# Kernel tuning notes

Measured on AMD Instinct MI355X. Metric: run time of the kernel, lower is better.

Reference implementation:

```python
import jax, jax.numpy as jnp
import numpy as np

# Config (matches init_kwargs)
N_HEAD, D_K, D_MODEL, D_INNER, N_LAYERS = 8, 64, 512, 2048, 4
VOCAB, PAD_IDX, REP_IDX, N_POSITION = 512, 0, 1, 200
B, N_NEAR, S = 64, 32, 12  # B batches, 32 near-POIs each, <=12 type tokens per POI
NPOI = B * N_NEAR


def sinusoid_table(n_position, d):
    pos = np.arange(n_position)[:, None].astype(np.float64)
    i = np.arange(d)[None, :]
    angle = pos / np.power(10000.0, 2 * (i // 2) / d)
    tab = np.zeros((n_position, d))
    tab[:, 0::2] = np.sin(angle[:, 0::2])
    tab[:, 1::2] = np.cos(angle[:, 1::2])
    return jnp.asarray(tab, jnp.float32)


def layer_norm(x, g, b, eps=1e-6):
    m = jnp.mean(x, -1, keepdims=True)
    v = jnp.var(x, -1, keepdims=True)
    return g * (x - m) * jax.lax.rsqrt(v + eps) + b


def pack_indices(npl, ttn):
    """Replace the torch Python-loop ragged pack with a single precomputed gather.
    Returns per-output-slot (poi_idx, tok_idx) and a validity mask [B, L]."""
    npl = np.asarray(npl); ttn = np.asarray(ttn)
    Bn = len(npl)
    ends = np.cumsum(npl); starts = ends - npl
    seq_len = np.array([1 + int(ttn[starts[b]:ends[b]].sum()) for b in range(Bn)])
    L = int(seq_len.max())  # == max_batch_len in the torch code
    poi_idx = np.zeros((Bn, L), np.int32)
    tok_idx = np.zeros((Bn, L), np.int32)
    for b in range(Bn):
        pos = 1  # slot 0 is the [REP] token
        for p in range(int(starts[b]), int(ends[b])):
            t = int(ttn[p])
            poi_idx[b, pos:pos + t] = p
            tok_idx[b, pos:pos + t] = np.arange(t)
            pos += t
    valid = np.arange(L)[None, :] < seq_len[:, None]  # pad_from_num_list(pad_num)
    return poi_idx, tok_idx, valid


def setup_inputs() -> dict:
    key = jax.random.key(0)
    ks = jax.random.split(key, 24)
    nrm = lambda k, shape, s=0.02: jax.random.normal(k, shape, jnp.float32) * s
    poi_type = jax.random.randint(ks[0], (NPOI, S), 0, VOCAB, jnp.int32)
    loc_emb = jax.random.normal(ks[1], (NPOI, D_MODEL), jnp.float32)
    near_pois_num_list = jnp.full((B,), N_NEAR, jnp.int32)
    type_token_num = jax.random.randint(ks[2], (NPOI,), 1, S + 1, jnp.int32)
    emb = nrm(ks[3], (VOCAB, D_MODEL), 1.0).at[PAD_IDX].set(0.0)  # padding_idx row zeroed
    return {
        "poi_type": poi_type, "loc_emb": loc_emb,
        "near_pois_num_list": near_pois_num_list, "type_token_num": type_token_num,
        "emb": emb,
        "Wq": nrm(ks[4], (N_LAYERS, D_MODEL, D_MODEL)),
        "Wk": nrm(ks[5], (N_LAYERS, D_MODEL, D_MODEL)),
        "Wv": nrm(ks[6], (N_LAYERS, D_MODEL, D_MODEL)),
        "Wo": nrm(ks[7], (N_LAYERS, D_MODEL, D_MODEL)),
        "bo": jnp.zeros((N_LAYERS, D_MODEL), jnp.float32),
        "ln1_g": jnp.ones((N_LAYERS, D_MODEL), jnp.float32),
        "ln1_b": jnp.zeros((N_LAYERS, D_MODEL), jnp.float32),
        "W1": nrm(ks[8], (N_LAYERS, D_MODEL, D_INNER)),
        "b1": jnp.zeros((N_LAYERS, D_INNER), jnp.float32),
        "W2": nrm(ks[9], (N_LAYERS, D_INNER, D_MODEL)),
        "b2": jnp.zeros((N_LAYERS, D_MODEL), jnp.float32),
        "ln2_g": jnp.ones((N_LAYERS, D_MODEL), jnp.float32),
        "ln2_b": jnp.zeros((N_LAYERS, D_MODEL), jnp.float32),
        "lnf_g": jnp.ones((D_MODEL,), jnp.float32),
        "lnf_b": jnp.zeros((D_MODEL,), jnp.float32),
    }


def encoder_forward(poi_type, loc_emb, poi_idx, tok_idx, tok_mask, attn_mask,
                    emb, Wq, Wk, Wv, Wo, bo, ln1_g, ln1_b, W1, b1, W2, b2,
                    ln2_g, ln2_b, lnf_g, lnf_b):
    pos_table = sinusoid_table(N_POSITION, D_MODEL)
    # embedding + positional encoding (dropout = eval/identity) + location broadcast
    enc = emb[poi_type] + pos_table[None, :S, :] + loc_emb[:, None, :]  # [NPOI, S, D]
    # fused ragged gather+pad (replaces the per-row torch.cat loop)
    x = jnp.where(tok_mask[..., None], enc[poi_idx, tok_idx], 0.0)      # [B, L, D]
    x = x.at[:, 0, :].set(emb[REP_IDX])                                  # [REP] token at slot 0
    x = layer_norm(x, lnf_g, lnf_b)
    Bn, L, D = x.shape
    inv_temp = np.float32(1.0 / np.sqrt(D_K))
    for l in range(N_LAYERS):
        # multi-head self-attention, post-LN residual
        q = (x @ Wq[l]).reshape(Bn, L, N_HEAD, D_K)
        k = (x @ Wk[l]).reshape(Bn, L, N_HEAD, D_K)
        v = (x @ Wv[l]).reshape(Bn, L, N_HEAD, D_K)
        scores = jnp.einsum('bqhd,bkhd->bhqk', q, k) * inv_temp
        scores = jnp.where(attn_mask[:, None, None, :], scores, -1e9)
        attn = jax.nn.softmax(scores, axis=-1)
        o = jnp.einsum('bhqk,bkhd->bqhd', attn, v).reshape(Bn, L, D)
        x = layer_norm(x + o @ Wo[l] + bo[l], ln1_g[l], ln1_b[l])
        # position-wise FFN, post-LN residual
        h = jax.nn.relu(x @ W1[l] + b1[l])
        x = layer_norm(x + h @ W2[l] + b2[l], ln2_g[l], ln2_b[l])
    return x


def reference(poi_type, loc_emb, near_pois_num_list, type_token_num,
              emb, Wq, Wk, Wv, Wo, bo, ln1_g, ln1_b, W1, b1, W2, b2,
              ln2_g, ln2_b, lnf_g, lnf_b):
    poi_idx, tok_idx, valid = pack_indices(np.asarray(near_pois_num_list),
                                           np.asarray(type_token_num))
    L = valid.shape[1]
    tok_mask = jnp.asarray(valid & (np.arange(L)[None, :] > 0))
    attn_mask = jnp.asarray(valid)
    out = encoder_forward(poi_type, loc_emb, jnp.asarray(poi_idx), jnp.asarray(tok_idx),
                          tok_mask, attn_mask, emb, Wq, Wk, Wv, Wo, bo,
                          ln1_g, ln1_b, W1, b1, W2, b2, ln2_g, ln2_b, lnf_g, lnf_b)
    return out, attn_mask
```

## Files before the change

### kernel.cpp

```cpp
#include <hip/hip_runtime.h>
#include <stdint.h>

#define DM 512
#define NH 8
#define DKH 64
#define DI 2048
#define NLAY 4
#define SMAX 12
#define BATCH 64
#define NPOI 2048
#define REPIDX 1
#define VOCAB 512

#define PLS 40

#define S_POI 0
#define S_LOC 1
#define S_NPL 2
#define S_TTN 3
#define S_EMB 4
#define S_WQ 5
#define S_WK 6
#define S_WV 7
#define S_WO 8
#define S_BO 9
#define S_LN1G 10
#define S_LN1B 11
#define S_W1 12
#define S_B1 13
#define S_W2 14
#define S_B2 15
#define S_LN2G 16
#define S_LN2B 17
#define S_LNFG 18
#define S_LNFB 19

#define F_FD 0
#define F_SI 1

typedef unsigned short u16;
typedef short short8 __attribute__((ext_vector_type(8)));
typedef float f32x4 __attribute__((ext_vector_type(4)));
typedef const uint32_t __attribute__((address_space(1)))* as1_u32p;
typedef uint32_t __attribute__((address_space(3)))* as3_u32p;

__device__ __forceinline__ float bf2f(u16 u) {
    union { uint32_t i; float f; } v; v.i = (uint32_t)u << 16; return v.f;
}
__device__ __forceinline__ u16 f2bf(float f) {
    union { uint32_t i; float f; } v; v.f = f;
    uint32_t u = v.i;
    u += 0x7fffu + ((u >> 16) & 1u);
    return (u16)(u >> 16);
}
__device__ __forceinline__ float loadIn(const void* p, size_t i, int fd) {
    if (fd == 1) return bf2f(((const u16*)p)[i]);
    if (fd == 3) { union { u16 u; _Float16 h; } v; v.u = ((const u16*)p)[i]; return (float)v.h; }
    if (fd == 2) return (float)((const double*)p)[i];
    return ((const float*)p)[i];
}
__device__ __forceinline__ int loadInt(const void* p, size_t i, int istride) {
    return (int)((const uint32_t*)p)[i * istride];
}

__global__ void bind_kernel(void* a0, void* a1, void* a2, void* a3, void* a4,
                            void* c0, void* c1, void* c2, void* c3, void* c4, void* c5, void* c6,
                            void* f0, void* f1,
                            void* w40, void* w41,
                            void* poi, void* npl, void* emb, void* b1,
                            void** tab, int* flags) {
    if (threadIdx.x != 0 || blockIdx.x != 0) return;

    int fd = -1, gAt = -1;
    {
        const u16* a16 = (const u16*)f0; const uint32_t* a32 = (const uint32_t*)f0;
        const unsigned long long* a64 = (const unsigned long long*)f0;
        if (a16[0] == 0x3C00 && a16[1] == 0x3C00) { fd = 3; gAt = 0; }
        else if (a16[0] == 0x3F80 && a16[1] == 0x3F80) { fd = 1; gAt = 0; }
        else if (a32[0] == 0x3F800000u) { fd = 0; gAt = 0; }
        else if (a64[0] == 0x3FF0000000000000ull) { fd = 2; gAt = 0; }
        else {
            const u16* b16 = (const u16*)f1; const uint32_t* b32 = (const uint32_t*)f1;
            const unsigned long long* b64 = (const unsigned long long*)f1;
            if (b16[0] == 0x3C00 && b16[1] == 0x3C00) { fd = 3; gAt = 1; }
            else if (b16[0] == 0x3F80 && b16[1] == 0x3F80) { fd = 1; gAt = 1; }
            else if (b32[0] == 0x3F800000u) { fd = 0; gAt = 1; }
            else if (b64[0] == 0x3FF0000000000000ull) { fd = 2; gAt = 1; }
        }
        if (fd < 0) { fd = 0; gAt = 0; }
    }

    int sI = 1;
    {
        const uint32_t* n32 = (const uint32_t*)npl;
        if (n32[0] == 32u && n32[1] == 0u && n32[2] == 32u) sI = 2;
    }

    void* g1[5] = {a0, a1, a2, a3, a4};
    int locIdx = -1;
    for (int j = 0; j < 5 && locIdx < 0; ++j) {
        float mx = 0.f;
        for (int s = 0; s < 64; ++s) {
            float v = loadIn(g1[j], (size_t)s * 997 + 13, fd);
            mx = fmaxf(mx, fabsf(v));
        }
        if (mx > 0.5f) locIdx = j;
    }
    if (locIdx < 0) locIdx = 0;
    tab[S_LOC] = g1[locIdx];
    {
        int wslot[4] = {S_WQ, S_WK, S_WV, S_WO}; int wi = 0;
        for (int j = 0; j < 5; ++j) if (j != locIdx) tab[wslot[wi++]] = g1[j];
    }

    void* g2[7] = {c0, c1, c2, c3, c4, c5, c6};
    int ttnIdx = -1;
    for (int j = 0; j < 7 && ttnIdx < 0; ++j) {
        const uint32_t* u = (const uint32_t*)g2[j];
        bool ok = true;
        for (int s = 0; s < 24; ++s) {
            uint32_t lo = u[(size_t)s * sI];
            if (lo < 1u || lo > 12u) { ok = false; break; }
            if (sI == 2 && u[(size_t)s * 2 + 1] != 0u) { ok = false; break; }
        }
        if (ok) ttnIdx = j;
    }
    if (ttnIdx < 0) ttnIdx = 0;
    tab[S_TTN] = g2[ttnIdx];
    {
        int gslots[2] = {S_LN1G, S_LN2G}; int bslots[4] = {S_BO, S_LN1B, S_B2, S_LN2B};
        int gi = 0, bi = 0;
        for (int j = 0; j < 7; ++j) {
            if (j == ttnIdx) continue;
            float v0 = loadIn(g2[j], 0, fd);
            if (v0 > 0.5f && gi < 2) tab[gslots[gi++]] = g2[j];
            else if (bi < 4) tab[bslots[bi++]] = g2[j];
            else if (gi < 2) tab[gslots[gi++]] = g2[j];
        }
    }

    tab[S_LNFG] = gAt == 0 ? f0 : f1;
    tab[S_LNFB] = gAt == 0 ? f1 : f0;
    tab[S_W1] = w40; tab[S_W2] = w41;
    tab[S_POI] = poi; tab[S_NPL] = npl; tab[S_EMB] = emb; tab[S_B1] = b1;

    flags[F_FD] = fd;
    flags[F_SI] = sI;
}

__global__ void bind_positional(void* p0, void* p1, void* p2, void* p3, void* p4,
                                void* p5, void* p6, void* p7, void* p8, void* p9,
                                void* p10, void* p11, void* p12, void* p13, void* p14,
                                void* p15, void* p16, void* p17, void* p18, void* p19,
                                void** tab, int* flags) {
    if (threadIdx.x != 0) return;
    void* ps[20] = {p0,p1,p2,p3,p4,p5,p6,p7,p8,p9,p10,p11,p12,p13,p14,p15,p16,p17,p18,p19};
    for (int i = 0; i < 20; ++i) tab[i] = ps[i];
    flags[F_FD] = 0; flags[F_SI] = 1;
}

__global__ void sinusoid_kernel(float* __restrict__ tab) {
    int i = blockIdx.x * 256 + threadIdx.x;
    if (i >= SMAX * DM) return;
    int s = i / DM, d = i - s * DM;
    double expo = (double)(2 * (d / 2)) / (double)DM;
    double angle = (double)s / pow(10000.0, expo);
    tab[i] = (float)((d & 1) ? cos(angle) : sin(angle));
}

__global__ void pack_kernel(void* const* tab, const int* flags,
                            int* __restrict__ seq_len, int* __restrict__ poi_idx,
                            int* __restrict__ tok_idx, int L) {
    const void* npl = tab[S_NPL];
    const void* ttn = tab[S_TTN];
    const int sI = flags[F_SI];
    int b = threadIdx.x;
    if (b >= BATCH) return;
    int start = 0;
    for (int i = 0; i < b; ++i) start += loadInt(npl, i, sI);
    int cnt = loadInt(npl, b, sI);
    for (int j = 0; j < L; ++j) { poi_idx[b * L + j] = 0; tok_idx[b * L + j] = 0; }
    int pos = 1;
    for (int p = start; p < start + cnt; ++p) {
        int tn = loadInt(ttn, p, sI);
        for (int j = 0; j < tn; ++j) {
            if (pos < L) { poi_idx[b * L + pos] = p; tok_idx[b * L + pos] = j; ++pos; }
        }
    }
    seq_len[b] = pos;
}

__global__ __launch_bounds__(256) void build_enc(void* const* tab, const int* flags,
                                                 const float* __restrict__ pos_tab,
                                                 float* __restrict__ enc) {
    const int fd = flags[F_FD], sI = flags[F_SI];
    const void* poi_type = tab[S_POI];
    const void* loc_emb = tab[S_LOC];
    const void* emb = tab[S_EMB];
    int ps = blockIdx.x;
    int p = ps / SMAX, s = ps - p * SMAX;
    int tok = loadInt(poi_type, ps, sI);
    tok = tok < 0 ? 0 : (tok >= VOCAB ? VOCAB - 1 : tok);
    #pragma unroll
    for (int j = 0; j < 2; ++j) {
        int d = threadIdx.x + 256 * j;
        enc[(size_t)ps * DM + d] = loadIn(emb, (size_t)tok * DM + d, fd)
                                 + pos_tab[s * DM + d]
                                 + loadIn(loc_emb, (size_t)p * DM + d, fd);
    }
}

__global__ __launch_bounds__(64) void gather_ln_wave(void* const* tab, const int* flags,
                                                     const float* __restrict__ enc,
                                                     const int* __restrict__ poi_idx,
                                                     const int* __restrict__ tok_idx,
                                                     const int* __restrict__ seq_len,
                                                     float* __restrict__ x, u16* __restrict__ xb,
                                                     int L) {
    const int fd = flags[F_FD];
    const void* emb = tab[S_EMB];
    const void* g = tab[S_LNFG];
    const void* bb = tab[S_LNFB];
    const int row = blockIdx.x;
    const int b = row / L, l = row - b * L;
    const int lane = threadIdx.x;
    const int slen = seq_len[b];
    float e[8];
    if (l == 0) {
        #pragma unroll
        for (int j = 0; j < 8; ++j) e[j] = loadIn(emb, REPIDX * DM + lane + 64 * j, fd);
    } else if (l < slen) {
        int p = poi_idx[row];
        p = p < 0 ? 0 : (p >= NPOI ? NPOI - 1 : p);
        int t = tok_idx[row];
        t = t < 0 ? 0 : (t >= SMAX ? SMAX - 1 : t);
        const float* src = enc + ((size_t)p * SMAX + t) * DM;
        #pragma unroll
        for (int j = 0; j < 8; ++j) e[j] = src[lane + 64 * j];
    } else {
        #pragma unroll
        for (int j = 0; j < 8; ++j) e[j] = 0.f;
    }
    float s1 = 0.f, s2 = 0.f;
    #pragma unroll
    for (int j = 0; j < 8; ++j) { s1 += e[j]; s2 += e[j] * e[j]; }
    #pragma unroll
    for (int off = 1; off < 64; off <<= 1) {
        s1 += __shfl_xor(s1, off, 64);
        s2 += __shfl_xor(s2, off, 64);
    }
    float mean = s1 * (1.f / DM);
    float var = s2 * (1.f / DM) - mean * mean;
    float rs = rsqrtf(fmaxf(var, 0.f) + 1e-6f);
    #pragma unroll
    for (int j = 0; j < 8; ++j) {
        int d = lane + 64 * j;
        float o = loadIn(g, d, fd) * (e[j] - mean) * rs + loadIn(bb, d, fd);
        x[(size_t)row * DM + d] = o;
        xb[(size_t)row * DM + d] = f2bf(o);
    }
}

__global__ __launch_bounds__(64) void ln_wave(void* const* tab, const int* flags,
                                              float* __restrict__ x, const u16* __restrict__ t,
                                              int gslot, int bslot, int poff,
                                              u16* __restrict__ xb) {
    const int fd = flags[F_FD];
    const void* g = tab[gslot];
    const void* bb = tab[bslot];
    const int row = blockIdx.x;
    const int lane = threadIdx.x;
    float e[8];
    #pragma unroll
    for (int j = 0; j < 8; ++j) {
        int d = lane + 64 * j;
        e[j] = x[(size_t)row * DM + d] + bf2f(t[(size_t)row * DM + d]);
    }
    float s1 = 0.f, s2 = 0.f;
    #pragma unroll
    for (int j = 0; j < 8; ++j) { s1 += e[j]; s2 += e[j] * e[j]; }
    #pragma unroll
    for (int off = 1; off < 64; off <<= 1) {
        s1 += __shfl_xor(s1, off, 64);
        s2 += __shfl_xor(s2, off, 64);
    }
    float mean = s1 * (1.f / DM);
    float var = s2 * (1.f / DM) - mean * mean;
    float rs = rsqrtf(fmaxf(var, 0.f) + 1e-6f);
    #pragma unroll
    for (int j = 0; j < 8; ++j) {
        int d = lane + 64 * j;
        float o = loadIn(g, poff + d, fd) * (e[j] - mean) * rs + loadIn(bb, poff + d, fd);
        x[(size_t)row * DM + d] = o;
        xb[(size_t)row * DM + d] = f2bf(o);
    }
}

__global__ __launch_bounds__(256) void transpose_tiled(void* const* tab, const int* flags,
                                                       int srcslot, u16* __restrict__ dst,
                                                       int K, int N,
                                                       size_t srcStride, size_t dstStride) {
    __shared__ float ts[32][33];
    const int fd = flags[F_FD];
    const void* src = tab[srcslot];
    const int layer = blockIdx.y;
    const size_t soff = (size_t)layer * srcStride;
    u16* d = dst + (size_t)layer * dstStride;
    const int ntx = N >> 5;
    const int kt = blockIdx.x / ntx, nt = blockIdx.x - kt * ntx;
    const int tx = threadIdx.x & 31, ty = threadIdx.x >> 5;
    #pragma unroll
    for (int j = 0; j < 4; ++j)
        ts[ty + j * 8][tx] = loadIn(src, soff + (size_t)(kt * 32 + ty + j * 8) * N + nt * 32 + tx, fd);
    __syncthreads();
    #pragma unroll
    for (int j = 0; j < 4; ++j)
        d[(size_t)(nt * 32 + ty + j * 8) * K + kt * 32 + tx] = f2bf(ts[tx][ty + j * 8]);
}

__global__ void zero_u16(u16* __restrict__ p, int n) {
    int i = blockIdx.x * 256 + threadIdx.x;
    if (i < n) p[i] = 0;
}
__global__ void zero_vt(u16* __restrict__ vt, int L, int Lr) {
    int tail = Lr - L;
    int n = BATCH * DM * tail;
    int i = blockIdx.x * 256 + threadIdx.x;
    if (i < n) {
        int rd = i / tail;
        int kk = L + (i - rd * tail);
        vt[(size_t)rd * Lr + kk] = 0;
    }
}

template <bool RELU>
__global__ __launch_bounds__(256) void gemm_mfma(const u16* __restrict__ A, const u16* __restrict__ Bt,
                                                 void* const* tab, const int* flags,
                                                 int biasslot, int boff,
                                                 u16* __restrict__ C, int N, int K) {
    __shared__ __align__(16) u16 As[128 * 32];
    __shared__ __align__(16) u16 Bs[128 * 32];
    const int tid = threadIdx.x;
    const int lane = tid & 63;
    const int w = tid >> 6;
    const int wr = w >> 1, wc = w & 1;
    const int m0 = blockIdx.x * 128, n0 = blockIdx.y * 128;

    const int sr = tid >> 2;
    const int sc = (tid & 3) * 8;
    u16* a0dst = As + w * 512;
    u16* a1dst = As + 2048 + w * 512;
    u16* b0dst = Bs + w * 512;
    u16* b1dst = Bs + 2048 + w * 512;

    const int row_in = lane & 15;
    const int k8 = (lane >> 4) * 8;

    f32x4 acc[4][4];
    const f32x4 fz = {0.f, 0.f, 0.f, 0.f};
    #pragma unroll
    for (int i = 0; i < 4; ++i)
        #pragma unroll
        for (int j = 0; j < 4; ++j) acc[i][j] = fz;

    for (int k0 = 0; k0 < K; k0 += 32) {
        __syncthreads();
        __builtin_amdgcn_global_load_lds((as1_u32p)(const void*)(A + (size_t)(m0 + sr) * K + k0 + sc),
                                         (as3_u32p)(void*)a0dst, 16, 0, 0);
        __builtin_amdgcn_global_load_lds((as1_u32p)(const void*)(A + (size_t)(m0 + sr + 64) * K + k0 + sc),
                                         (as3_u32p)(void*)a1dst, 16, 0, 0);
        __builtin_amdgcn_global_load_lds((as1_u32p)(const void*)(Bt + (size_t)(n0 + sr) * K + k0 + sc),
                                         (as3_u32p)(void*)b0dst, 16, 0, 0);
        __builtin_amdgcn_global_load_lds((as1_u32p)(const void*)(Bt + (size_t)(n0 + sr + 64) * K + k0 + sc),
                                         (as3_u32p)(void*)b1dst, 16, 0, 0);
        __syncthreads();

        short8 af[4], bfr[4];
        #pragma unroll
        for (int mf = 0; mf < 4; ++mf)
            af[mf] = *(const short8*)&As[(wr * 64 + mf * 16 + row_in) * 32 + k8];
        #pragma unroll
        for (int nf = 0; nf < 4; ++nf)
            bfr[nf] = *(const short8*)&Bs[(wc * 64 + nf * 16 + row_in) * 32 + k8];
        #pragma unroll
        for (int mf = 0; mf < 4; ++mf)
            #pragma unroll
            for (int nf = 0; nf < 4; ++nf)
                acc[mf][nf] = __builtin_amdgcn_mfma_f32_16x16x32_bf16(af[mf], bfr[nf], acc[mf][nf], 0, 0, 0);
    }

    const int fd = flags[F_FD];
    #pragma unroll
    for (int nf = 0; nf < 4; ++nf) {
        int col = n0 + wc * 64 + nf * 16 + (lane & 15);
        float bv = (biasslot >= 0) ? loadIn(tab[biasslot], boff + col, fd) : 0.f;
        #pragma unroll
        for (int mf = 0; mf < 4; ++mf) {
            int rbase = m0 + wr * 64 + mf * 16 + (lane >> 4) * 4;
            #pragma unroll
            for (int r = 0; r < 4; ++r) {
                float v = acc[mf][nf][r] + bv;
                if (RELU) v = v > 0.f ? v : 0.f;
                C[(size_t)(rbase + r) * N + col] = f2bf(v);
            }
        }
    }
}

__global__ __launch_bounds__(256) void gemm_qkv(const u16* __restrict__ A, const u16* __restrict__ Bt,
                                                u16* __restrict__ qk, u16* __restrict__ vt,
                                                int L, int Lr, int M, int Mp) {
    __shared__ __align__(16) u16 As[128 * 32];
    __shared__ __align__(16) u16 Bs[128 * 32];
    const int tid = threadIdx.x;
    const int lane = tid & 63;
    const int w = tid >> 6;
    const int wr = w >> 1, wc = w & 1;
    const int m0 = blockIdx.x * 128, n0 = blockIdx.y * 128;

    const int sr = tid >> 2;
    const int sc = (tid & 3) * 8;
    u16* a0dst = As + w * 512;
    u16* a1dst = As + 2048 + w * 512;
    u16* b0dst = Bs + w * 512;
    u16* b1dst = Bs + 2048 + w * 512;

    const int row_in = lane & 15;
    const int k8 = (lane >> 4) * 8;

    f32x4 acc[4][4];
    const f32x4 fz = {0.f, 0.f, 0.f, 0.f};
    #pragma unroll
    for (int i = 0; i < 4; ++i)
        #pragma unroll
        for (int j = 0; j < 4; ++j) acc[i][j] = fz;

    for (int k0 = 0; k0 < DM; k0 += 32) {
        __syncthreads();
        __builtin_amdgcn_global_load_lds((as1_u32p)(const void*)(A + (size_t)(m0 + sr) * DM + k0 + sc),
                                         (as3_u32p)(void*)a0dst, 16, 0, 0);
        __builtin_amdgcn_global_load_lds((as1_u32p)(const void*)(A + (size_t)(m0 + sr + 64) * DM + k0 + sc),
                                         (as3_u32p)(void*)a1dst, 16, 0, 0);
        __builtin_amdgcn_global_load_lds((as1_u32p)(const void*)(Bt + (size_t)(n0 + sr) * DM + k0 + sc),
                                         (as3_u32p)(void*)b0dst, 16, 0, 0);
        __builtin_amdgcn_global_load_lds((as1_u32p)(const void*)(Bt + (size_t)(n0 + sr + 64) * DM + k0 + sc),
                                         (as3_u32p)(void*)b1dst, 16, 0, 0);
        __syncthreads();

        short8 af[4], bfr[4];
        #pragma unroll
        for (int mf = 0; mf < 4; ++mf)
            af[mf] = *(const short8*)&As[(wr * 64 + mf * 16 + row_in) * 32 + k8];
        #pragma unroll
        for (int nf = 0; nf < 4; ++nf)
            bfr[nf] = *(const short8*)&Bs[(wc * 64 + nf * 16 + row_in) * 32 + k8];
        #pragma unroll
        for (int mf = 0; mf < 4; ++mf)
            #pragma unroll
            for (int nf = 0; nf < 4; ++nf)
                acc[mf][nf] = __builtin_amdgcn_mfma_f32_16x16x32_bf16(af[mf], bfr[nf], acc[mf][nf], 0, 0, 0);
    }

    const size_t MpDM = (size_t)Mp * DM;
    #pragma unroll
    for (int mf = 0; mf < 4; ++mf) {
        #pragma unroll
        for (int r = 0; r < 4; ++r) {
            int row = m0 + wr * 64 + mf * 16 + (lane >> 4) * 4 + r;
            int bb2 = row / L;
            int ltok = row - bb2 * L;
            #pragma unroll
            for (int nf = 0; nf < 4; ++nf) {
                int col = n0 + wc * 64 + nf * 16 + (lane & 15);
                float v = acc[mf][nf][r];
                if (col < 1024) {
                    qk[(size_t)(col >> 9) * MpDM + (size_t)row * DM + (col & 511)] = f2bf(v);
                } else if (row < M) {
                    vt[((size_t)bb2 * DM + (col - 1024)) * Lr + ltok] = f2bf(v);
                }
            }
        }
    }
}

__global__ __launch_bounds__(64) void attn_flash(const u16* __restrict__ q, const u16* __restrict__ k,
                                                 const u16* __restrict__ vt, u16* __restrict__ o,
                                                 const int* __restrict__ seq_len, int L, int Lr, int M) {
    __shared__ __align__(16) u16 pl[16 * PLS];
    const int lane = threadIdx.x;
    const int qt = blockIdx.x, h = blockIdx.y, b = blockIdx.z;
    const int slen = seq_len[b];
    const size_t base = (size_t)b * L;
    const int hcol = h * DKH;
    const int nk = (L + 15) >> 4;
    const int col = lane & 15;
    const int hi = lane >> 4;
    const int k8 = hi * 8;

    size_t qrr = base + qt * 16 + col;
    if (qrr >= (size_t)M) qrr = (size_t)M - 1;
    const short8 qf0 = *(const short8*)&q[qrr * DM + hcol + k8];
    const short8 qf1 = *(const short8*)&q[qrr * DM + hcol + 32 + k8];

    const u16* vbase = vt + ((size_t)b * DM + hcol) * Lr;

    f32x4 oacc[4];
    #pragma unroll
    for (int dt = 0; dt < 4; ++dt) oacc[dt] = (f32x4){0.f, 0.f, 0.f, 0.f};
    float m[4] = {-1e30f, -1e30f, -1e30f, -1e30f};
    float ll[4] = {0.f, 0.f, 0.f, 0.f};

    const int nchunk = (nk + 1) >> 1;
    for (int c = 0; c < nchunk; ++c) {
        const int kt0 = c * 2, kt1 = c * 2 + 1;
        f32x4 s0, s1;
        {
            size_t krr = base + kt0 * 16 + col;
            if (krr >= (size_t)M) krr = (size_t)M - 1;
            short8 kf0 = *(const short8*)&k[krr * DM + hcol + k8];
            short8 kf1 = *(const short8*)&k[krr * DM + hcol + 32 + k8];
            f32x4 a = {0.f, 0.f, 0.f, 0.f};
            a = __builtin_amdgcn_mfma_f32_16x16x32_bf16(qf0, kf0, a, 0, 0, 0);
            a = __builtin_amdgcn_mfma_f32_16x16x32_bf16(qf1, kf1, a, 0, 0, 0);
            s0 = a;
        }
        {
            size_t krr = base + kt1 * 16 + col;
            if (krr >= (size_t)M) krr = (size_t)M - 1;
            short8 kf0 = *(const short8*)&k[krr * DM + hcol + k8];
            short8 kf1 = *(const short8*)&k[krr * DM + hcol + 32 + k8];
            f32x4 a = {0.f, 0.f, 0.f, 0.f};
            a = __builtin_amdgcn_mfma_f32_16x16x32_bf16(qf0, kf0, a, 0, 0, 0);
            a = __builtin_amdgcn_mfma_f32_16x16x32_bf16(qf1, kf1, a, 0, 0, 0);
            s1 = a;
        }
        const bool v0 = (kt0 * 16 + col) < slen;
        const bool v1 = (kt1 < nk) && ((kt1 * 16 + col) < slen);
        float cm[4];
        #pragma unroll
        for (int r = 0; r < 4; ++r) {
            float a0 = v0 ? s0[r] * 0.125f : -1e30f;
            float a1 = v1 ? s1[r] * 0.125f : -1e30f;
            s0[r] = a0; s1[r] = a1;
            cm[r] = fmaxf(a0, a1);
        }
        #pragma unroll
        for (int r = 0; r < 4; ++r) {
            #pragma unroll
            for (int off = 1; off < 16; off <<= 1)
                cm[r] = fmaxf(cm[r], __shfl_xor(cm[r], off, 64));
        }
        float scr[4];
        #pragma unroll
        for (int r = 0; r < 4; ++r) {
            float nm = fmaxf(m[r], cm[r]);
            scr[r] = __expf(m[r] - nm);
            m[r] = nm;
        }
        #pragma unroll
        for (int dt = 0; dt < 4; ++dt)
            #pragma unroll
            for (int r = 0; r < 4; ++r) oacc[dt][r] *= scr[r];
        #pragma unroll
        for (int r = 0; r < 4; ++r) {
            float p0 = __expf(s0[r] - m[r]);
            float p1 = __expf(s1[r] - m[r]);
            ll[r] = ll[r] * scr[r] + p0 + p1;
            pl[(hi * 4 + r) * PLS + col] = f2bf(p0);
            pl[(hi * 4 + r) * PLS + 16 + col] = f2bf(p1);
        }
        __syncthreads();
        short8 pa = *(const short8*)&pl[col * PLS + k8];
        #pragma unroll
        for (int dt = 0; dt < 4; ++dt) {
            short8 vf = *(const short8*)&vbase[(size_t)(dt * 16 + col) * Lr + c * 32 + k8];
            oacc[dt] = __builtin_amdgcn_mfma_f32_16x16x32_bf16(pa, vf, oacc[dt], 0, 0, 0);
        }
        __syncthreads();
    }

    #pragma unroll
    for (int r = 0; r < 4; ++r) {
        #pragma unroll
        for (int off = 1; off < 16; off <<= 1)
            ll[r] += __shfl_xor(ll[r], off, 64);
    }
    #pragma unroll
    for (int r = 0; r < 4; ++r) {
        int qr = qt * 16 + hi * 4 + r;
        if (qr < L) {
            float inv = 1.f / ll[r];
            #pragma unroll
            for (int dt = 0; dt < 4; ++dt)
                o[(base + qr) * DM + hcol + dt * 16 + col] = f2bf(oacc[dt][r] * inv);
        }
    }
}

__global__ void store_out(const float* __restrict__ x, float* __restrict__ out, int n) {
    int i = blockIdx.x * 256 + threadIdx.x;
    if (i < n) out[i] = x[i];
}
__global__ void store_mask(const int* __restrict__ seq_len, float* __restrict__ out, int L, int M) {
    int i = blockIdx.x * 256 + threadIdx.x;
    if (i < M) {
        int b = i / L, l = i - b * L;
        out[i] = (l < seq_len[b]) ? 1.0f : 0.0f;
    }
}

extern "C" void kernel_launch(void* const* d_in, const int* in_sizes, int n_in,
                              void* d_out, int out_size, void* d_ws, size_t ws_size,
                              hipStream_t stream) {
    const int L = out_size / (BATCH * (DM + 1));
    const int M = BATCH * L;
    const int Mp = (M + 127) & ~127;
    const int Lr = (L + 31) & ~31;
    const int nk = (L + 15) >> 4;

    uint8_t* p = (uint8_t*)d_ws;
    auto carve = [&](size_t bytes) -> void* {
        void* r = (void*)p;
        p += (bytes + 255) & ~(size_t)255;
        return r;
    };
    void** tab = (void**)carve(20 * sizeof(void*));
    int* flags = (int*)carve(8 * 4);
    int* seq_len = (int*)carve((size_t)BATCH * 4);
    int* poi_idx = (int*)carve((size_t)M * 4);
    int* tok_idx = (int*)carve((size_t)M * 4);
    float* pos_tab = (float*)carve((size_t)SMAX * DM * 4);
    float* x = (float*)carve((size_t)Mp * DM * 4);
    u16* t = (u16*)carve((size_t)Mp * DM * 2);
    u16* xb = (u16*)carve((size_t)Mp * DM * 2);
    const size_t MpDM = (size_t)Mp * DM;
    const size_t vt_bytes = (size_t)BATCH * DM * Lr * 2;
    size_t region_bytes = (size_t)Mp * DI * 2;
    size_t qkv_bytes = 3 * MpDM * 2 + vt_bytes;
    size_t enc_bytes = (size_t)NPOI * SMAX * DM * 4;
    if (qkv_bytes > region_bytes) region_bytes = qkv_bytes;
    if (enc_bytes > region_bytes) region_bytes = enc_bytes;
    u16* region = (u16*)carve(region_bytes);
    const size_t SQ = (size_t)DM * DM;
    const size_t SF = (size_t)DM * DI;
    const size_t PST = 4 * SQ + 2 * SF;
    u16* WT4 = (u16*)carve(PST * NLAY * 2);

    float* enc = (float*)region;
    u16* qb = region;
    u16* kb = region + MpDM;
    u16* ob = region + 2 * MpDM;
    u16* vt = region + 3 * MpDM;

    int g1M[8], n1M = 0, g2k[8], n2k = 0, g4M[4], n4M = 0, g512[4], n512 = 0;
    int idx_poi = -1, idx_npl = -1, idx_emb = -1, idx_b1 = -1;
    int cpoi = 0, cnpl = 0, cemb = 0, cb1 = 0;
    for (int i = 0; i < n_in; ++i) {
        switch (in_sizes[i]) {
            case 24576: idx_poi = i; ++cpoi; break;
            case 64: idx_npl = i; ++cnpl; break;
            case 262144: idx_emb = i; ++cemb; break;
            case 8192: idx_b1 = i; ++cb1; break;
            case 1048576: if (n1M < 8) g1M[n1M] = i; ++n1M; break;
            case 2048: if (n2k < 8) g2k[n2k] = i; ++n2k; break;
            case 4194304: if (n4M < 4) g4M[n4M] = i; ++n4M; break;
            case 512: if (n512 < 4) g512[n512] = i; ++n512; break;
            default: break;
        }
    }
    bool census = (n_in == 20) && cpoi == 1 && cnpl == 1 && cemb == 1 && cb1 == 1 &&
                  n1M == 5 && n2k == 7 && n4M == 2 && n512 == 2;

    if (census) {
        bind_kernel<<<1, 1, 0, stream>>>(
            d_in[g1M[0]], d_in[g1M[1]], d_in[g1M[2]], d_in[g1M[3]], d_in[g1M[4]],
            d_in[g2k[0]], d_in[g2k[1]], d_in[g2k[2]], d_in[g2k[3]], d_in[g2k[4]], d_in[g2k[5]], d_in[g2k[6]],
            d_in[g512[0]], d_in[g512[1]],
            d_in[g4M[0]], d_in[g4M[1]],
            d_in[idx_poi], d_in[idx_npl], d_in[idx_emb], d_in[idx_b1],
            tab, flags);
    } else {
        void* q[20];
        for (int i = 0; i < 20; ++i) q[i] = (i < n_in) ? d_in[i] : d_in[0];
        bind_positional<<<1, 1, 0, stream>>>(q[0], q[1], q[2], q[3], q[4], q[5], q[6], q[7], q[8], q[9],
                                             q[10], q[11], q[12], q[13], q[14], q[15], q[16], q[17], q[18], q[19],
                                             tab, flags);
    }

    sinusoid_kernel<<<(SMAX * DM + 255) / 256, 256, 0, stream>>>(pos_tab);
    pack_kernel<<<1, 64, 0, stream>>>(tab, flags, seq_len, poi_idx, tok_idx, L);
    build_enc<<<NPOI * SMAX, 256, 0, stream>>>(tab, flags, pos_tab, enc);
    gather_ln_wave<<<M, 64, 0, stream>>>(tab, flags, enc, poi_idx, tok_idx, seq_len, x, xb, L);
    if (Mp > M) {
        int nz = (Mp - M) * DM;
        zero_u16<<<(nz + 255) / 256, 256, 0, stream>>>(xb + (size_t)M * DM, nz);
    }

    {
        dim3 gTQ(16 * 16, NLAY);
        transpose_tiled<<<gTQ, 256, 0, stream>>>(tab, flags, S_WQ, WT4,            DM, DM, SQ, PST);
        transpose_tiled<<<gTQ, 256, 0, stream>>>(tab, flags, S_WK, WT4 + SQ,       DM, DM, SQ, PST);
        transpose_tiled<<<gTQ, 256, 0, stream>>>(tab, flags, S_WV, WT4 + 2 * SQ,   DM, DM, SQ, PST);
        transpose_tiled<<<gTQ, 256, 0, stream>>>(tab, flags, S_WO, WT4 + 3 * SQ,   DM, DM, SQ, PST);
        dim3 gT1(16 * 64, NLAY);
        transpose_tiled<<<gT1, 256, 0, stream>>>(tab, flags, S_W1, WT4 + 4 * SQ,   DM, DI, SF, PST);
        dim3 gT2(64 * 16, NLAY);
        transpose_tiled<<<gT2, 256, 0, stream>>>(tab, flags, S_W2, WT4 + 4 * SQ + SF, DI, DM, SF, PST);
    }

    dim3 gP(Mp / 128, DM / 128);
    dim3 gQKV(Mp / 128, 1536 / 128);
    dim3 gF(Mp / 128, DI / 128);
    dim3 gAF(nk, NH, BATCH);
    const int vtTail = (Lr - L) * BATCH * DM;
    for (int l = 0; l < NLAY; ++l) {
        u16* WL = WT4 + (size_t)l * PST;
        if (Lr > L)
            zero_vt<<<(vtTail + 255) / 256, 256, 0, stream>>>(vt, L, Lr);
        gemm_qkv<<<gQKV, 256, 0, stream>>>(xb, WL, region, vt, L, Lr, M, Mp);
        attn_flash<<<gAF, 64, 0, stream>>>(qb, kb, vt, ob, seq_len, L, Lr, M);
        gemm_mfma<false><<<gP, 256, 0, stream>>>(ob, WL + 3 * SQ, tab, flags, S_BO, l * DM, t, DM, DM);
        ln_wave<<<M, 64, 0, stream>>>(tab, flags, x, t, S_LN1G, S_LN1B, l * DM, xb);
        gemm_mfma<true><<<gF, 256, 0, stream>>>(xb, WL + 4 * SQ, tab, flags, S_B1, l * DI, region, DI, DM);
        gemm_mfma<false><<<gP, 256, 0, stream>>>(region, WL + 4 * SQ + SF, tab, flags, S_B2, l * DM, t, DM, DI);
        ln_wave<<<M, 64, 0, stream>>>(tab, flags, x, t, S_LN2G, S_LN2B, l * DM, xb);
    }

    float* out = (float*)d_out;
    store_out<<<(M * DM + 255) / 256, 256, 0, stream>>>(x, out, M * DM);
    store_mask<<<(M + 255) / 256, 256, 0, stream>>>(seq_len, out + (size_t)M * DM, L, M);
}
```

Before: 1.582 ms.

## Double-buffer GEMM LDS tiles, add XCD-aware block swizzle, pack four LN rows per block

```diff
diff --git a/kernel.cpp b/kernel.cpp
--- a/kernel.cpp
+++ b/kernel.cpp
@@ -63,6 +63,12 @@
     return (int)((const uint32_t*)p)[i * istride];
 }
 
+__device__ __forceinline__ int xcd_swizzle(int lin, int nwg) {
+    int qq = nwg >> 3, rr = nwg & 7;
+    int xcd = lin & 7, off = lin >> 3;
+    return (xcd < rr ? xcd * (qq + 1) : rr * (qq + 1) + (xcd - rr) * qq) + off;
+}
+
 __global__ void bind_kernel(void* a0, void* a1, void* a2, void* a3, void* a4,
                             void* c0, void* c1, void* c2, void* c3, void* c4, void* c5, void* c6,
                             void* f0, void* f1,
@@ -261,15 +267,16 @@
     }
 }
 
-__global__ __launch_bounds__(64) void ln_wave(void* const* tab, const int* flags,
-                                              float* __restrict__ x, const u16* __restrict__ t,
-                                              int gslot, int bslot, int poff,
-                                              u16* __restrict__ xb) {
+__global__ __launch_bounds__(256) void ln_wave(void* const* tab, const int* flags,
+                                               float* __restrict__ x, const u16* __restrict__ t,
+                                               int gslot, int bslot, int poff,
+                                               u16* __restrict__ xb, int M) {
     const int fd = flags[F_FD];
     const void* g = tab[gslot];
     const void* bb = tab[bslot];
-    const int row = blockIdx.x;
-    const int lane = threadIdx.x;
+    const int row = blockIdx.x * 4 + (threadIdx.x >> 6);
+    if (row >= M) return;
+    const int lane = threadIdx.x & 63;
     float e[8];
     #pragma unroll
     for (int j = 0; j < 8; ++j) {
@@ -338,24 +345,32 @@
                                                  void* const* tab, const int* flags,
                                                  int biasslot, int boff,
                                                  u16* __restrict__ C, int N, int K) {
-    __shared__ __align__(16) u16 As[128 * 32];
-    __shared__ __align__(16) u16 Bs[128 * 32];
+    __shared__ __align__(16) u16 As[2][128 * 32];
+    __shared__ __align__(16) u16 Bs[2][128 * 32];
     const int tid = threadIdx.x;
     const int lane = tid & 63;
     const int w = tid >> 6;
     const int wr = w >> 1, wc = w & 1;
-    const int m0 = blockIdx.x * 128, n0 = blockIdx.y * 128;
+    const int gx = gridDim.x;
+    int lin = xcd_swizzle(blockIdx.x + gx * blockIdx.y, gx * gridDim.y);
+    const int m0 = (lin % gx) * 128, n0 = (lin / gx) * 128;
 
     const int sr = tid >> 2;
     const int sc = (tid & 3) * 8;
-    u16* a0dst = As + w * 512;
-    u16* a1dst = As + 2048 + w * 512;
-    u16* b0dst = Bs + w * 512;
-    u16* b1dst = Bs + 2048 + w * 512;
-
     const int row_in = lane & 15;
     const int k8 = (lane >> 4) * 8;
 
+    auto STAGE = [&](int buf, int k0) {
+        __builtin_amdgcn_global_load_lds((as1_u32p)(const void*)(A + (size_t)(m0 + sr) * K + k0 + sc),
+                                         (as3_u32p)(void*)(As[buf] + w * 512), 16, 0, 0);
+        __builtin_amdgcn_global_load_lds((as1_u32p)(const void*)(A + (size_t)(m0 + sr + 64) * K + k0 + sc),
+                                         (as3_u32p)(void*)(As[buf] + 2048 + w * 512), 16, 0, 0);
+        __builtin_amdgcn_global_load_lds((as1_u32p)(const void*)(Bt + (size_t)(n0 + sr) * K + k0 + sc),
+                                         (as3_u32p)(void*)(Bs[buf] + w * 512), 16, 0, 0);
+        __builtin_amdgcn_global_load_lds((as1_u32p)(const void*)(Bt + (size_t)(n0 + sr + 64) * K + k0 + sc),
+                                         (as3_u32p)(void*)(Bs[buf] + 2048 + w * 512), 16, 0, 0);
+    };
+
     f32x4 acc[4][4];
     const f32x4 fz = {0.f, 0.f, 0.f, 0.f};
     #pragma unroll
@@ -363,30 +378,26 @@
         #pragma unroll
         for (int j = 0; j < 4; ++j) acc[i][j] = fz;
 
-    for (int k0 = 0; k0 < K; k0 += 32) {
-        __syncthreads();
-        __builtin_amdgcn_global_load_lds((as1_u32p)(const void*)(A + (size_t)(m0 + sr) * K + k0 + sc),
-                                         (as3_u32p)(void*)a0dst, 16, 0, 0);
-        __builtin_amdgcn_global_load_lds((as1_u32p)(const void*)(A + (size_t)(m0 + sr + 64) * K + k0 + sc),
-                                         (as3_u32p)(void*)a1dst, 16, 0, 0);
-        __builtin_amdgcn_global_load_lds((as1_u32p)(const void*)(Bt + (size_t)(n0 + sr) * K + k0 + sc),
-                                         (as3_u32p)(void*)b0dst, 16, 0, 0);
-        __builtin_amdgcn_global_load_lds((as1_u32p)(const void*)(Bt + (size_t)(n0 + sr + 64) * K + k0 + sc),
-                                         (as3_u32p)(void*)b1dst, 16, 0, 0);
-        __syncthreads();
-
+    const int nt = K >> 5;
+    STAGE(0, 0);
+    __syncthreads();
+    int cur = 0;
+    for (int t = 0; t < nt; ++t) {
+        if (t + 1 < nt) STAGE(cur ^ 1, (t + 1) * 32);
         short8 af[4], bfr[4];
         #pragma unroll
         for (int mf = 0; mf < 4; ++mf)
-            af[mf] = *(const short8*)&As[(wr * 64 + mf * 16 + row_in) * 32 + k8];
+            af[mf] = *(const short8*)&As[cur][(wr * 64 + mf * 16 + row_in) * 32 + k8];
         #pragma unroll
         for (int nf = 0; nf < 4; ++nf)
-            bfr[nf] = *(const short8*)&Bs[(wc * 64 + nf * 16 + row_in) * 32 + k8];
+            bfr[nf] = *(const short8*)&Bs[cur][(wc * 64 + nf * 16 + row_in) * 32 + k8];
         #pragma unroll
         for (int mf = 0; mf < 4; ++mf)
             #pragma unroll
             for (int nf = 0; nf < 4; ++nf)
                 acc[mf][nf] = __builtin_amdgcn_mfma_f32_16x16x32_bf16(af[mf], bfr[nf], acc[mf][nf], 0, 0, 0);
+        __syncthreads();
+        cur ^= 1;
     }
 
     const int fd = flags[F_FD];
@@ -410,24 +421,32 @@
 __global__ __launch_bounds__(256) void gemm_qkv(const u16* __restrict__ A, const u16* __restrict__ Bt,
                                                 u16* __restrict__ qk, u16* __restrict__ vt,
                                                 int L, int Lr, int M, int Mp) {
-    __shared__ __align__(16) u16 As[128 * 32];
-    __shared__ __align__(16) u16 Bs[128 * 32];
+    __shared__ __align__(16) u16 As[2][128 * 32];
+    __shared__ __align__(16) u16 Bs[2][128 * 32];
     const int tid = threadIdx.x;
     const int lane = tid & 63;
     const int w = tid >> 6;
     const int wr = w >> 1, wc = w & 1;
-    const int m0 = blockIdx.x * 128, n0 = blockIdx.y * 128;
+    const int gx = gridDim.x;
+    int lin = xcd_swizzle(blockIdx.x + gx * blockIdx.y, gx * gridDim.y);
+    const int m0 = (lin % gx) * 128, n0 = (lin / gx) * 128;
 
     const int sr = tid >> 2;
     const int sc = (tid & 3) * 8;
-    u16* a0dst = As + w * 512;
-    u16* a1dst = As + 2048 + w * 512;
-    u16* b0dst = Bs + w * 512;
-    u16* b1dst = Bs + 2048 + w * 512;
-
     const int row_in = lane & 15;
     const int k8 = (lane >> 4) * 8;
 
+    auto STAGE = [&](int buf, int k0) {
+        __builtin_amdgcn_global_load_lds((as1_u32p)(const void*)(A + (size_t)(m0 + sr) * DM + k0 + sc),
+                                         (as3_u32p)(void*)(As[buf] + w * 512), 16, 0, 0);
+        __builtin_amdgcn_global_load_lds((as1_u32p)(const void*)(A + (size_t)(m0 + sr + 64) * DM + k0 + sc),
+                                         (as3_u32p)(void*)(As[buf] + 2048 + w * 512), 16, 0, 0);
+        __builtin_amdgcn_global_load_lds((as1_u32p)(const void*)(Bt + (size_t)(n0 + sr) * DM + k0 + sc),
+                                         (as3_u32p)(void*)(Bs[buf] + w * 512), 16, 0, 0);
+        __builtin_amdgcn_global_load_lds((as1_u32p)(const void*)(Bt + (size_t)(n0 + sr + 64) * DM + k0 + sc),
+                                         (as3_u32p)(void*)(Bs[buf] + 2048 + w * 512), 16, 0, 0);
+    };
+
     f32x4 acc[4][4];
     const f32x4 fz = {0.f, 0.f, 0.f, 0.f};
     #pragma unroll
@@ -435,30 +454,26 @@
         #pragma unroll
         for (int j = 0; j < 4; ++j) acc[i][j] = fz;
 
-    for (int k0 = 0; k0 < DM; k0 += 32) {
-        __syncthreads();
-        __builtin_amdgcn_global_load_lds((as1_u32p)(const void*)(A + (size_t)(m0 + sr) * DM + k0 + sc),
-                                         (as3_u32p)(void*)a0dst, 16, 0, 0);
-        __builtin_amdgcn_global_load_lds((as1_u32p)(const void*)(A + (size_t)(m0 + sr + 64) * DM + k0 + sc),
-                                         (as3_u32p)(void*)a1dst, 16, 0, 0);
-        __builtin_amdgcn_global_load_lds((as1_u32p)(const void*)(Bt + (size_t)(n0 + sr) * DM + k0 + sc),
-                                         (as3_u32p)(void*)b0dst, 16, 0, 0);
-        __builtin_amdgcn_global_load_lds((as1_u32p)(const void*)(Bt + (size_t)(n0 + sr + 64) * DM + k0 + sc),
-                                         (as3_u32p)(void*)b1dst, 16, 0, 0);
-        __syncthreads();
-
+    const int nt = DM >> 5;
+    STAGE(0, 0);
+    __syncthreads();
+    int cur = 0;
+    for (int t = 0; t < nt; ++t) {
+        if (t + 1 < nt) STAGE(cur ^ 1, (t + 1) * 32);
         short8 af[4], bfr[4];
         #pragma unroll
         for (int mf = 0; mf < 4; ++mf)
-            af[mf] = *(const short8*)&As[(wr * 64 + mf * 16 + row_in) * 32 + k8];
+            af[mf] = *(const short8*)&As[cur][(wr * 64 + mf * 16 + row_in) * 32 + k8];
         #pragma unroll
         for (int nf = 0; nf < 4; ++nf)
-            bfr[nf] = *(const short8*)&Bs[(wc * 64 + nf * 16 + row_in) * 32 + k8];
+            bfr[nf] = *(const short8*)&Bs[cur][(wc * 64 + nf * 16 + row_in) * 32 + k8];
         #pragma unroll
         for (int mf = 0; mf < 4; ++mf)
             #pragma unroll
             for (int nf = 0; nf < 4; ++nf)
                 acc[mf][nf] = __builtin_amdgcn_mfma_f32_16x16x32_bf16(af[mf], bfr[nf], acc[mf][nf], 0, 0, 0);
+        __syncthreads();
+        cur ^= 1;
     }
 
     const size_t MpDM = (size_t)Mp * DM;
@@ -711,6 +726,7 @@
     dim3 gP(Mp / 128, DM / 128);
     dim3 gQKV(Mp / 128, 1536 / 128);
     dim3 gF(Mp / 128, DI / 128);
+    dim3 gLN((M + 3) / 4);
     dim3 gAF(nk, NH, BATCH);
     const int vtTail = (Lr - L) * BATCH * DM;
     for (int l = 0; l < NLAY; ++l) {
@@ -720,10 +736,10 @@
         gemm_qkv<<<gQKV, 256, 0, stream>>>(xb, WL, region, vt, L, Lr, M, Mp);
         attn_flash<<<gAF, 64, 0, stream>>>(qb, kb, vt, ob, seq_len, L, Lr, M);
         gemm_mfma<false><<<gP, 256, 0, stream>>>(ob, WL + 3 * SQ, tab, flags, S_BO, l * DM, t, DM, DM);
-        ln_wave<<<M, 64, 0, stream>>>(tab, flags, x, t, S_LN1G, S_LN1B, l * DM, xb);
+        ln_wave<<<gLN, 256, 0, stream>>>(tab, flags, x, t, S_LN1G, S_LN1B, l * DM, xb, M);
         gemm_mfma<true><<<gF, 256, 0, stream>>>(xb, WL + 4 * SQ, tab, flags, S_B1, l * DI, region, DI, DM);
         gemm_mfma<false><<<gP, 256, 0, stream>>>(region, WL + 4 * SQ + SF, tab, flags, S_B2, l * DM, t, DM, DI);
-        ln_wave<<<M, 64, 0, stream>>>(tab, flags, x, t, S_LN2G, S_LN2B, l * DM, xb);
+        ln_wave<<<gLN, 256, 0, stream>>>(tab, flags, x, t, S_LN2G, S_LN2B, l * DM, xb, M);
     }
 
     float* out = (float*)d_out;
```

Result: no change. 1.595 ms (+0.8%).
